# Optimization experiments

Hardware: AMD Instinct MI355X
Metric: run time of the kernel (lower is better)

The kernel has to match this reference:

```python
import jax, jax.numpy as jnp
import numpy as np

COST_CLASS = 1.0
COST_MASK = 1.0
COST_DICE = 1.0


def setup_inputs() -> dict:
    key = jax.random.key(0)
    k1, k2, k3, k4 = jax.random.split(key, 4)
    B, Q, G, T, L = 16, 100, 16384, 50, 21
    masks_queries_logits = jax.random.normal(k1, (B, Q, G), dtype=jnp.float32)
    class_queries_logits = jax.random.normal(k2, (B, Q, L), dtype=jnp.float32)
    mask_labels = (jax.random.uniform(k3, (B, T, G)) < 0.1).astype(jnp.float32)
    class_labels = jax.random.randint(k4, (B, T), 0, L, dtype=jnp.int64)
    return {
        "masks_queries_logits": masks_queries_logits,
        "class_queries_logits": class_queries_logits,
        "mask_labels": mask_labels,
        "class_labels": class_labels,
    }


def reference(masks_queries_logits, class_queries_logits, mask_labels, class_labels):
    """Returns the [B, Q, T] Hungarian cost matrices (the GPU-side compute of the
    matcher). The scipy linear_sum_assignment step is CPU-side and excluded."""
    G = masks_queries_logits.shape[-1]
    L = class_queries_logits.shape[-1]

    # classification cost: -softmax(pred)[:, target_class]
    probs = jax.nn.softmax(class_queries_logits, axis=-1)          # [B,Q,L]
    onehot = jax.nn.one_hot(class_labels, L, dtype=probs.dtype)    # [B,T,L]
    cost_class = -jnp.einsum('bql,btl->bqt', probs, onehot)        # [B,Q,T]

    # pairwise sigmoid cross-entropy cost (BCE-with-logits vs target 1 / target 0)
    ce_pos = jax.nn.softplus(-masks_queries_logits)                # [B,Q,G]
    ce_neg = jax.nn.softplus(masks_queries_logits)                 # [B,Q,G]
    cost_mask = (jnp.einsum('bqg,btg->bqt', ce_pos, mask_labels)
                 + jnp.einsum('bqg,btg->bqt', ce_neg, 1.0 - mask_labels)) / G

    # pairwise dice cost
    sig = jax.nn.sigmoid(masks_queries_logits)                     # [B,Q,G]
    numerator = 2.0 * jnp.einsum('bqg,btg->bqt', sig, mask_labels)
    denominator = sig.sum(-1)[:, :, None] + mask_labels.sum(-1)[:, None, :]
    cost_dice = 1.0 - (numerator + 1.0) / (denominator + 1.0)

    return COST_MASK * cost_mask + COST_CLASS * cost_class + COST_DICE * cost_dice
```

## Files before the change

kernel.cpp:

```cpp
#include <hip/hip_runtime.h>
#include <stdint.h>

#define NB 16
#define NQ 100
#define QP 112
#define NG 16384
#define NT 50
#define TP 64
#define NL 21
#define CH 256
#define NCHUNK (NG/CH)

#define OFF_SSP  0u
#define SZ_SSP   (NB*QP*4u)
#define OFF_DOTM (OFF_SSP + SZ_SSP)
#define SZ_DOT   ((size_t)NB*QP*TP*4u)
#define OFF_DOTS (OFF_DOTM + SZ_DOT)
#define ZERO_SZ  (OFF_DOTS + SZ_DOT)

typedef __bf16 bf16x8 __attribute__((ext_vector_type(8)));
typedef float f32x4 __attribute__((ext_vector_type(4)));
union Frag { uint32_t u[4]; bf16x8 v; };

__device__ __forceinline__ uint32_t pack_bf16(float a, float b) {
  uint32_t ua = __float_as_uint(a), ub = __float_as_uint(b);
  ua = (ua + 0x7FFFu + ((ua >> 16) & 1u)) >> 16;
  ub = (ub + 0x7FFFu + ((ub >> 16) & 1u)) & 0xFFFF0000u;
  return ua | ub;
}

__device__ __forceinline__ uint32_t cvtpk(float a, float b) {
  uint32_t r;
  asm("v_cvt_pk_bf16_f32 %0, %1, %2" : "=v"(r) : "v"(a), "v"(b));
  return r;
}

__global__ __launch_bounds__(448, 7) void fused_main(
    const float* __restrict__ m, const float* __restrict__ mask,
    float* __restrict__ ssp, float* __restrict__ dotm,
    float* __restrict__ dots) {
  __shared__ __align__(16) uint32_t bfr[8 * 4 * 64 * 4];
  int blk = blockIdx.x;
  int chunk = blk & (NCHUNK - 1), b = blk >> 6;
  int tid = threadIdx.x;

  {
    int sub = tid & 7, tb = tid >> 3;
    uint2* U2 = (uint2*)bfr;
    int half = sub & 1;
    int lgs = sub >> 1;
    for (int t = tb; t < 64; t += 56) {
      int nt = t >> 4;
      int l = lgs * 16 + (t & 15);
      if (t < NT) {
        const float* src = mask + ((size_t)(b*NT + t))*NG + chunk*CH + sub*4;
#pragma unroll
        for (int i = 0; i < 8; ++i) {
          float4 f = *(const float4*)(src + i*32);
          uint2 pk;
          pk.x = pack_bf16(f.x, f.y);
          pk.y = pack_bf16(f.z, f.w);
          U2[((i*4 + nt)*64 + l)*2 + half] = pk;
        }
      } else {
        uint32_t c = (t == 63) ? 0x3F803F80u : 0u;
        uint2 pk; pk.x = c; pk.y = c;
#pragma unroll
        for (int i = 0; i < 8; ++i)
          U2[((i*4 + nt)*64 + l)*2 + half] = pk;
      }
    }
  }
  __syncthreads();

  int lane = tid & 63, wv = tid >> 6;
  int row16 = lane & 15, lg = lane >> 4;
  int q0 = wv * 16;
  int qrow = q0 + row16;
  bool pad = qrow > NQ - 1;
  int qc = pad ? NQ - 1 : qrow;
  const float* arow = m + (size_t)(b*NQ + qc)*NG + chunk*CH + lg*8;
  const bf16x8* BF = (const bf16x8*)bfr;

  f32x4 accm[4], accs[4];
#pragma unroll
  for (int nt = 0; nt < 4; ++nt) { accm[nt] = (f32x4)(0.f); accs[nt] = (f32x4)(0.f); }
  float sl = 0.f;

#pragma unroll 2
  for (int ks = 0; ks < 8; ++ks) {
    const float4* p = (const float4*)(arow + ks*32);
    float4 v0 = p[0], v1 = p[1];
    float av[8] = {v0.x, v0.y, v0.z, v0.w, v1.x, v1.y, v1.z, v1.w};
    Frag mf, sf;
#pragma unroll
    for (int j = 0; j < 8; j += 2) {
      float x0 = av[j], x1 = av[j+1];
      x0 = pad ? 1.f : x0;
      x1 = pad ? 1.f : x1;
      float e0 = __builtin_amdgcn_exp2f(x0 * -1.442695041f);
      float e1 = __builtin_amdgcn_exp2f(x1 * -1.442695041f);
      float u0 = 1.f + e0, u1 = 1.f + e1;
      float r0 = __builtin_amdgcn_rcpf(u0), r1 = __builtin_amdgcn_rcpf(u1);
      sl += __builtin_amdgcn_logf(u0) + __builtin_amdgcn_logf(u1);
      mf.u[j >> 1] = cvtpk(x0, x1);
      sf.u[j >> 1] = cvtpk(r0, r1);
    }
#pragma unroll
    for (int nt = 0; nt < 4; ++nt) {
      bf16x8 bb = BF[(ks*4 + nt)*64 + lane];
      accm[nt] = __builtin_amdgcn_mfma_f32_16x16x32_bf16(mf.v, bb, accm[nt], 0, 0, 0);
      accs[nt] = __builtin_amdgcn_mfma_f32_16x16x32_bf16(sf.v, bb, accs[nt], 0, 0, 0);
    }
  }

  sl += __shfl_xor(sl, 16); sl += __shfl_xor(sl, 32);
  if (lg == 0) atomicAdd(&ssp[b*QP + q0 + row16], sl);

#pragma unroll
  for (int nt = 0; nt < 4; ++nt) {
    int t = nt*16 + row16;
#pragma unroll
    for (int r = 0; r < 4; ++r) {
      int qq = q0 + lg*4 + r;
      atomicAdd(&dotm[(size_t)(b*QP + qq)*TP + t], accm[nt][r]);
      atomicAdd(&dots[(size_t)(b*QP + qq)*TP + t], accs[nt][r]);
    }
  }
}

__global__ __launch_bounds__(64) void finalize_k(
    const float* __restrict__ cls, const int* __restrict__ labels,
    const float* __restrict__ ssp, const float* __restrict__ dotm,
    const float* __restrict__ dots, float* __restrict__ out) {
  int blk = blockIdx.x;
  int b = blk / NQ, q = blk % NQ;
  int lane = threadIdx.x;
  const float* lgt = cls + (size_t)(b*NQ + q) * NL;
  float v = (lane < NL) ? lgt[lane] : -1e30f;
  float mx = v;
  for (int s = 32; s; s >>= 1) mx = fmaxf(mx, __shfl_xor(mx, s));
  float e = (lane < NL) ? __expf(v - mx) : 0.f;
  float se = e;
  for (int s = 32; s; s >>= 1) se += __shfl_xor(se, s);

  if (lane < NT) {
    int lbl = labels[b*NT + lane];
    float p = __expf(lgt[lbl] - mx) / se;
    size_t base = (size_t)(b*QP + q) * TP;
    float s1 = dotm[base + 63] + 0.69314718056f * ssp[b*QP + q];
    float sg = dots[base + 63];
    float msum = dotm[(size_t)(b*QP + 111)*TP + lane];
    float dm = dotm[base + lane];
    float ds = dots[base + lane];
    float cmask = (s1 - dm) * (1.f / (float)NG);
    float cdice = 1.f - (2.f*ds + 1.f) / (sg + msum + 1.f);
    out[(size_t)(b*NQ + q)*NT + lane] = cmask - p + cdice;
  }
}

extern "C" void kernel_launch(void* const* d_in, const int* in_sizes, int n_in,
                              void* d_out, int out_size, void* d_ws, size_t ws_size,
                              hipStream_t stream) {
  const float* mq = (const float*)d_in[0];
  const float* cq = (const float*)d_in[1];
  const float* ml = (const float*)d_in[2];
  const int*   cl = (const int*)d_in[3];
  char* ws = (char*)d_ws;
  float* ssp  = (float*)(ws + OFF_SSP);
  float* dotm = (float*)(ws + OFF_DOTM);
  float* dots = (float*)(ws + OFF_DOTS);

  hipMemsetAsync(ws, 0, ZERO_SZ, stream);
  fused_main<<<NB*NCHUNK, 448, 0, stream>>>(mq, ml, ssp, dotm, dots);
  finalize_k<<<NB*NQ, 64, 0, stream>>>(cq, cl, ssp, dotm, dots, (float*)d_out);
}
```

Measured before the change: 225.4 us.

## Replace atomic accumulation with per-chunk partial buffers and a separate reduce kernel

The GEMM kernel now writes per-chunk partial dot products straight to a workspace in MFMA fragment layout, replacing scattered float atomicAdds into the shared result. A new reduce kernel sums the chunk partials, and finalize reads through a fragment-aware index. The chunk size doubles to 512, so there are half as many blocks and each does twice the K loop. The inline cvt_pk asm is replaced by the software bf16 rounding helper. This removes atomic contention and the large memset, at the cost of an extra kernel launch and partial-buffer traffic.

Result: faster. 220.6 us (-2.1%).

```diff
diff --git a/kernel.cpp b/kernel.cpp
--- a/kernel.cpp
+++ b/kernel.cpp
@@ -8,15 +8,18 @@
 #define NT 50
 #define TP 64
 #define NL 21
-#define CH 256
-#define NCHUNK (NG/CH)
+#define NCH 32
+#define CH 512
 
-#define OFF_SSP  0u
+#define SZ_P     ((size_t)NCH*NB*7*1024*4)
+#define OFF_PM   0u
+#define OFF_PS   (SZ_P)
+#define OFF_RM   (2*SZ_P)
+#define SZ_R     ((size_t)NB*7*1024*4)
+#define OFF_RS   (OFF_RM + SZ_R)
+#define OFF_SSP  (OFF_RS + SZ_R)
 #define SZ_SSP   (NB*QP*4u)
-#define OFF_DOTM (OFF_SSP + SZ_SSP)
-#define SZ_DOT   ((size_t)NB*QP*TP*4u)
-#define OFF_DOTS (OFF_DOTM + SZ_DOT)
-#define ZERO_SZ  (OFF_DOTS + SZ_DOT)
+#define NEED_WS  (OFF_SSP + SZ_SSP)
 
 typedef __bf16 bf16x8 __attribute__((ext_vector_type(8)));
 typedef float f32x4 __attribute__((ext_vector_type(4)));
@@ -29,45 +32,38 @@
   return ua | ub;
 }
 
-__device__ __forceinline__ uint32_t cvtpk(float a, float b) {
-  uint32_t r;
-  asm("v_cvt_pk_bf16_f32 %0, %1, %2" : "=v"(r) : "v"(a), "v"(b));
-  return r;
-}
-
-__global__ __launch_bounds__(448, 7) void fused_main(
+__global__ __launch_bounds__(448) void gemm_part(
     const float* __restrict__ m, const float* __restrict__ mask,
-    float* __restrict__ ssp, float* __restrict__ dotm,
-    float* __restrict__ dots) {
-  __shared__ __align__(16) uint32_t bfr[8 * 4 * 64 * 4];
+    float* __restrict__ ssp, float* __restrict__ pdm,
+    float* __restrict__ pds) {
+  __shared__ __align__(16) uint32_t bfr[16 * 4 * 64 * 4];
   int blk = blockIdx.x;
-  int chunk = blk & (NCHUNK - 1), b = blk >> 6;
+  int chunk = blk & (NCH - 1), b = blk >> 5;
   int tid = threadIdx.x;
 
   {
-    int sub = tid & 7, tb = tid >> 3;
+    int sub = tid & 15, tb = tid >> 4;
     uint2* U2 = (uint2*)bfr;
-    int half = sub & 1;
-    int lgs = sub >> 1;
-    for (int t = tb; t < 64; t += 56) {
+    int lgs = (sub & 7) >> 1, half = sub & 1;
+    for (int t = tb; t < 64; t += 28) {
       int nt = t >> 4;
-      int l = lgs * 16 + (t & 15);
       if (t < NT) {
         const float* src = mask + ((size_t)(b*NT + t))*NG + chunk*CH + sub*4;
 #pragma unroll
         for (int i = 0; i < 8; ++i) {
-          float4 f = *(const float4*)(src + i*32);
-          uint2 pk;
-          pk.x = pack_bf16(f.x, f.y);
-          pk.y = pack_bf16(f.z, f.w);
-          U2[((i*4 + nt)*64 + l)*2 + half] = pk;
+          float4 f = *(const float4*)(src + i*64);
+          int ks = (sub >> 3) + i*2;
+          uint2 pk; pk.x = pack_bf16(f.x, f.y); pk.y = pack_bf16(f.z, f.w);
+          U2[((ks*4 + nt)*64 + lgs*16 + (t & 15))*2 + half] = pk;
         }
       } else {
         uint32_t c = (t == 63) ? 0x3F803F80u : 0u;
         uint2 pk; pk.x = c; pk.y = c;
 #pragma unroll
-        for (int i = 0; i < 8; ++i)
-          U2[((i*4 + nt)*64 + l)*2 + half] = pk;
+        for (int i = 0; i < 8; ++i) {
+          int ks = (sub >> 3) + i*2;
+          U2[((ks*4 + nt)*64 + lgs*16 + (t & 15))*2 + half] = pk;
+        }
       }
     }
   }
@@ -88,7 +84,7 @@
   float sl = 0.f;
 
 #pragma unroll 2
-  for (int ks = 0; ks < 8; ++ks) {
+  for (int ks = 0; ks < 16; ++ks) {
     const float4* p = (const float4*)(arow + ks*32);
     float4 v0 = p[0], v1 = p[1];
     float av[8] = {v0.x, v0.y, v0.z, v0.w, v1.x, v1.y, v1.z, v1.w};
@@ -103,8 +99,8 @@
       float u0 = 1.f + e0, u1 = 1.f + e1;
       float r0 = __builtin_amdgcn_rcpf(u0), r1 = __builtin_amdgcn_rcpf(u1);
       sl += __builtin_amdgcn_logf(u0) + __builtin_amdgcn_logf(u1);
-      mf.u[j >> 1] = cvtpk(x0, x1);
-      sf.u[j >> 1] = cvtpk(r0, r1);
+      mf.u[j >> 1] = pack_bf16(x0, x1);
+      sf.u[j >> 1] = pack_bf16(r0, r1);
     }
 #pragma unroll
     for (int nt = 0; nt < 4; ++nt) {
@@ -117,22 +113,39 @@
   sl += __shfl_xor(sl, 16); sl += __shfl_xor(sl, 32);
   if (lg == 0) atomicAdd(&ssp[b*QP + q0 + row16], sl);
 
+  size_t base = ((size_t)(b*NCH + chunk)*7 + wv)*1024 + lane*16;
 #pragma unroll
   for (int nt = 0; nt < 4; ++nt) {
-    int t = nt*16 + row16;
+    *(f32x4*)(pdm + base + nt*4) = accm[nt];
+    *(f32x4*)(pds + base + nt*4) = accs[nt];
+  }
+}
+
+__global__ __launch_bounds__(256) void reduce_k(
+    const float* __restrict__ pdm, const float* __restrict__ pds,
+    float* __restrict__ rm, float* __restrict__ rs) {
+  int idx = blockIdx.x*256 + threadIdx.x;
+  int b = idx / 7168, rem = idx % 7168;
+  size_t bp = (size_t)b*NCH*7168 + rem;
+  float sm = 0.f, ss = 0.f;
 #pragma unroll
-    for (int r = 0; r < 4; ++r) {
-      int qq = q0 + lg*4 + r;
-      atomicAdd(&dotm[(size_t)(b*QP + qq)*TP + t], accm[nt][r]);
-      atomicAdd(&dots[(size_t)(b*QP + qq)*TP + t], accs[nt][r]);
-    }
+  for (int ch = 0; ch < NCH; ++ch) {
+    sm += pdm[bp + (size_t)ch*7168];
+    ss += pds[bp + (size_t)ch*7168];
   }
+  rm[idx] = sm;
+  rs[idx] = ss;
+}
+
+__device__ __forceinline__ size_t ridx(int b, int q, int t) {
+  return (size_t)(b*7 + (q >> 4))*1024
+       + (size_t)((((q & 15) >> 2)*16 + (t & 15))*16 + (t >> 4)*4 + (q & 3));
 }
 
 __global__ __launch_bounds__(64) void finalize_k(
     const float* __restrict__ cls, const int* __restrict__ labels,
-    const float* __restrict__ ssp, const float* __restrict__ dotm,
-    const float* __restrict__ dots, float* __restrict__ out) {
+    const float* __restrict__ ssp, const float* __restrict__ rm,
+    const float* __restrict__ rs, float* __restrict__ out) {
   int blk = blockIdx.x;
   int b = blk / NQ, q = blk % NQ;
   int lane = threadIdx.x;
@@ -147,12 +160,11 @@
   if (lane < NT) {
     int lbl = labels[b*NT + lane];
     float p = __expf(lgt[lbl] - mx) / se;
-    size_t base = (size_t)(b*QP + q) * TP;
-    float s1 = dotm[base + 63] + 0.69314718056f * ssp[b*QP + q];
-    float sg = dots[base + 63];
-    float msum = dotm[(size_t)(b*QP + 111)*TP + lane];
-    float dm = dotm[base + lane];
-    float ds = dots[base + lane];
+    float s1 = rm[ridx(b, q, 63)] + 0.69314718056f * ssp[b*QP + q];
+    float sg = rs[ridx(b, q, 63)];
+    float msum = rm[ridx(b, 111, lane)];
+    float dm = rm[ridx(b, q, lane)];
+    float ds = rs[ridx(b, q, lane)];
     float cmask = (s1 - dm) * (1.f / (float)NG);
     float cdice = 1.f - (2.f*ds + 1.f) / (sg + msum + 1.f);
     out[(size_t)(b*NQ + q)*NT + lane] = cmask - p + cdice;
@@ -167,11 +179,14 @@
   const float* ml = (const float*)d_in[2];
   const int*   cl = (const int*)d_in[3];
   char* ws = (char*)d_ws;
-  float* ssp  = (float*)(ws + OFF_SSP);
-  float* dotm = (float*)(ws + OFF_DOTM);
-  float* dots = (float*)(ws + OFF_DOTS);
+  float* pdm = (float*)(ws + OFF_PM);
+  float* pds = (float*)(ws + OFF_PS);
+  float* rm  = (float*)(ws + OFF_RM);
+  float* rs  = (float*)(ws + OFF_RS);
+  float* ssp = (float*)(ws + OFF_SSP);
 
-  hipMemsetAsync(ws, 0, ZERO_SZ, stream);
-  fused_main<<<NB*NCHUNK, 448, 0, stream>>>(mq, ml, ssp, dotm, dots);
-  finalize_k<<<NB*NQ, 64, 0, stream>>>(cq, cl, ssp, dotm, dots, (float*)d_out);
+  hipMemsetAsync(ssp, 0, SZ_SSP, stream);
+  gemm_part<<<NB*NCH, 448, 0, stream>>>(mq, ml, ssp, pdm, pds);
+  reduce_k<<<448, 256, 0, stream>>>(pdm, pds, rm, rs);
+  finalize_k<<<NB*NQ, 64, 0, stream>>>(cq, cl, ssp, rm, rs, (float*)d_out);
 }
```
